# Kernel tuning notes

Measured on AMD Instinct MI355X. Metric: run time of the kernel, lower is better.

Reference implementation:

```python
import jax, jax.numpy as jnp
import numpy as np

N_NODES = 100000


def gcn_conv(x, src, dst, dinv, W, b):
    # PyG GCNConv: h = D^-1/2 (A+I) D^-1/2 (x W) + b
    h = x @ W                                   # [N, out]
    norm = dinv[src] * dinv[dst]                # [E'] edge weights
    msg = norm[:, None] * h[src]                # gather + scale
    agg = jax.ops.segment_sum(msg, dst, num_segments=x.shape[0])
    return agg + b


def setup_inputs() -> dict:
    key = jax.random.key(0)
    ks = jax.random.split(key, 8)
    x = jax.random.normal(ks[0], (N_NODES, 64), dtype=jnp.float32)
    edge_index = jax.random.randint(ks[1], (2, 1600000), 0, N_NODES, dtype=jnp.int32)
    s = 0.1
    return {
        "x": x,
        "edge_index": edge_index,
        "W1": jax.random.normal(ks[2], (64, 64), dtype=jnp.float32) * s,
        "b1": jnp.zeros((64,), dtype=jnp.float32),
        "W2": jax.random.normal(ks[3], (64, 32), dtype=jnp.float32) * s,
        "b2": jnp.zeros((32,), dtype=jnp.float32),
        "W3": jax.random.normal(ks[4], (32, 2), dtype=jnp.float32) * s,
        "b3": jnp.zeros((2,), dtype=jnp.float32),
    }


def reference(x, edge_index, W1, b1, W2, b2, W3, b3):
    n = x.shape[0]
    loop = jnp.arange(n, dtype=edge_index.dtype)
    src = jnp.concatenate([edge_index[0], loop])  # add self-loops
    dst = jnp.concatenate([edge_index[1], loop])
    deg = jax.ops.segment_sum(jnp.ones_like(dst, dtype=x.dtype), dst, num_segments=n)
    dinv = jnp.where(deg > 0, jax.lax.rsqrt(jnp.maximum(deg, 1.0)), 0.0)
    h = jax.nn.relu(gcn_conv(x, src, dst, dinv, W1, b1))
    h = jax.nn.relu(gcn_conv(h, src, dst, dinv, W2, b2))
    return gcn_conv(h, src, dst, dinv, W3, b3)
```

## Files before the change

kernel.cpp:

```cpp
#include <hip/hip_runtime.h>
#include <hip/hip_fp16.h>

#define N_NODES 100000
#define N_EDGES 1600000
#define BSHIFT 9
#define NBUCK ((N_NODES + 511) / 512)
#define BCAP 12288

__global__ void bucket1_kernel(const int* __restrict__ src, const int* __restrict__ dst,
                               int* __restrict__ gbcount, int2* __restrict__ bbuf, int E) {
    __shared__ int hcnt[NBUCK];
    __shared__ int hbase[NBUCK];
    int t = threadIdx.x;
    for (int i = t; i < NBUCK; i += 256) hcnt[i] = 0;
    __syncthreads();
    int e0 = blockIdx.x * 2048 + t;
    int ss[8], dd[8];
#pragma unroll
    for (int u = 0; u < 8; u++) {
        int e = e0 + u * 256;
        if (e < E) {
            ss[u] = src[e];
            dd[u] = dst[e];
            atomicAdd(&hcnt[dd[u] >> BSHIFT], 1);
        } else {
            dd[u] = -1;
        }
    }
    __syncthreads();
    for (int i = t; i < NBUCK; i += 256) {
        int c = hcnt[i];
        hbase[i] = c ? atomicAdd(&gbcount[i], c) : 0;
        hcnt[i] = 0;
    }
    __syncthreads();
#pragma unroll
    for (int u = 0; u < 8; u++) {
        if (dd[u] >= 0) {
            int bk = dd[u] >> BSHIFT;
            int r = atomicAdd(&hcnt[bk], 1);
            bbuf[(size_t)bk * BCAP + hbase[bk] + r] = make_int2(ss[u], dd[u]);
        }
    }
}

__global__ void scan196_kernel(const int* __restrict__ gbcount, int* __restrict__ gbase,
                               int* __restrict__ rowptrN, int E) {
    __shared__ int s[256];
    int t = threadIdx.x;
    int v = (t < NBUCK) ? gbcount[t] : 0;
    s[t] = v;
    __syncthreads();
    for (int off = 1; off < 256; off <<= 1) {
        int u = (t >= off) ? s[t - off] : 0;
        __syncthreads();
        s[t] += u;
        __syncthreads();
    }
    if (t < NBUCK) gbase[t] = s[t] - v;
    if (t == 0) *rowptrN = E;
}

__global__ __launch_bounds__(512)
void bucket2_kernel(const int2* __restrict__ bbuf, const int* __restrict__ gbcount,
                    const int* __restrict__ gbase, int* __restrict__ rowptr,
                    float* __restrict__ dinv, int* __restrict__ eidx, int N) {
    int b = blockIdx.x;
    int base_node = b << BSHIFT;
    int nn = min(512, N - base_node);
    int t = threadIdx.x;
    __shared__ int s[512];
    __shared__ int cur[512];
    s[t] = 0;
    __syncthreads();
    int sz = gbcount[b];
    const int2* eb = bbuf + (size_t)b * BCAP;
    for (int j = t; j < sz; j += 512) atomicAdd(&s[eb[j].y - base_node], 1);
    __syncthreads();
    int myc = s[t];
    if (t < nn) dinv[base_node + t] = rsqrtf((float)myc + 1.0f);
    __syncthreads();
    for (int off = 1; off < 512; off <<= 1) {
        int u = (t >= off) ? s[t - off] : 0;
        __syncthreads();
        s[t] += u;
        __syncthreads();
    }
    int rp = gbase[b] + s[t] - myc;
    if (t < nn) rowptr[base_node + t] = rp;
    cur[t] = rp;
    __syncthreads();
    for (int j = t; j < sz; j += 512) {
        int2 e = eb[j];
        int pos = atomicAdd(&cur[e.y - base_node], 1);
        eidx[pos] = e.x;
    }
}

__global__ void sortrow_wave(const int* __restrict__ rowptr, int* __restrict__ eidx, int n) {
    int g = (blockIdx.x * blockDim.x + threadIdx.x) >> 6;
    int lane = threadIdx.x & 63;
    if (g >= n) return;
    int start = rowptr[g];
    int end = rowptr[g + 1];
    int len = end - start;
    if (len <= 1) return;

    if (len <= 64) {
        int v = (lane < len) ? eidx[start + lane] : 0x7fffffff;
#pragma unroll
        for (int k = 2; k <= 64; k <<= 1) {
#pragma unroll
            for (int j = k >> 1; j > 0; j >>= 1) {
                int partner = __shfl_xor(v, j, 64);
                bool up = ((lane & k) == 0);
                bool keepMin = (((lane & j) == 0) == up);
                int mn = min(v, partner), mx = max(v, partner);
                v = keepMin ? mn : mx;
            }
        }
        if (lane < len) eidx[start + lane] = v;
    } else if (lane == 0) {
        for (int i = start + 1; i < end; i++) {
            int key = eidx[i];
            int j = i - 1;
            while (j >= start && eidx[j] > key) { eidx[j + 1] = eidx[j]; j--; }
            eidx[j + 1] = key;
        }
    }
}

template <int FIN, int FOUT, typename TO>
__global__ __launch_bounds__(256, 2)
void gemm_tiled(const float* __restrict__ in, const float* __restrict__ W,
                const float* __restrict__ dinv, TO* __restrict__ out, int n) {
    constexpr int CG = FOUT / 4;
    constexpr int RG = 256 / CG;
    constexpr int TR = RG * 4;
    constexpr int LDA = FIN + 4;
    __shared__ float sIn[TR * LDA];
    __shared__ float sW[FIN * FOUT];

    for (int i = threadIdx.x; i < FIN * FOUT / 4; i += 256)
        ((float4*)sW)[i] = ((const float4*)W)[i];

    int r0 = blockIdx.x * TR;
    for (int i = threadIdx.x; i < TR * FIN / 4; i += 256) {
        int rr = i / (FIN / 4);
        int cc = i % (FIN / 4);
        int gr = r0 + rr;
        float4 v = (gr < n) ? ((const float4*)in)[(size_t)gr * (FIN / 4) + cc]
                            : make_float4(0.f, 0.f, 0.f, 0.f);
        *(float4*)&sIn[rr * LDA + cc * 4] = v;
    }
    __syncthreads();

    int tc = threadIdx.x % CG;
    int tr = threadIdx.x / CG;
    int rbase = tr * 4, cbase = tc * 4;
    float acc[4][4] = {};

#pragma unroll 2
    for (int k = 0; k < FIN; k += 4) {
        float4 a[4], b[4];
#pragma unroll
        for (int i = 0; i < 4; i++) a[i] = *(float4*)&sIn[(rbase + i) * LDA + k];
#pragma unroll
        for (int kk = 0; kk < 4; kk++) b[kk] = *(float4*)&sW[(k + kk) * FOUT + cbase];
#pragma unroll
        for (int i = 0; i < 4; i++) {
            acc[i][0] += a[i].x * b[0].x + a[i].y * b[1].x + a[i].z * b[2].x + a[i].w * b[3].x;
            acc[i][1] += a[i].x * b[0].y + a[i].y * b[1].y + a[i].z * b[2].y + a[i].w * b[3].y;
            acc[i][2] += a[i].x * b[0].z + a[i].y * b[1].z + a[i].z * b[2].z + a[i].w * b[3].z;
            acc[i][3] += a[i].x * b[0].w + a[i].y * b[1].w + a[i].z * b[2].w + a[i].w * b[3].w;
        }
    }

#pragma unroll
    for (int i = 0; i < 4; i++) {
        int gr = r0 + rbase + i;
        if (gr < n) {
            float dv = dinv[gr];
            if constexpr (sizeof(TO) == 2) {
                union { __half h[4]; uint2 u; } pk;
                pk.h[0] = __float2half_rn(dv * acc[i][0]);
                pk.h[1] = __float2half_rn(dv * acc[i][1]);
                pk.h[2] = __float2half_rn(dv * acc[i][2]);
                pk.h[3] = __float2half_rn(dv * acc[i][3]);
                *(uint2*)&out[(size_t)gr * FOUT + cbase] = pk.u;
            } else {
                *(float4*)&out[(size_t)gr * FOUT + cbase] =
                    make_float4(dv * acc[i][0], dv * acc[i][1], dv * acc[i][2], dv * acc[i][3]);
            }
        }
    }
}

template <int FIN, int FOUT>
__global__ void gemm_kernel(const float* __restrict__ in, const float* __restrict__ W,
                            const float* __restrict__ dinv, float* __restrict__ out, int n) {
    __shared__ float sW[FIN * FOUT];
    for (int i = threadIdx.x; i < FIN * FOUT; i += blockDim.x) sW[i] = W[i];
    __syncthreads();
    constexpr int ROWS = 256 / FOUT;
    int r = blockIdx.x * ROWS + threadIdx.x / FOUT;
    int c = threadIdx.x % FOUT;
    if (r >= n) return;
    float acc = 0.f;
#pragma unroll
    for (int k = 0; k < FIN; k++) acc += in[r * FIN + k] * sW[k * FOUT + c];
    out[r * FOUT + c] = dinv[r] * acc;
}

template <int F, bool RELU>
__global__ void agg_h2_kernel(const int* __restrict__ eidx, const int* __restrict__ rowptr,
                              const float* __restrict__ dinv, const __half2* __restrict__ h2,
                              const float* __restrict__ b, float* __restrict__ out, int n) {
    constexpr int L = F / 2;
    int g = (blockIdx.x * blockDim.x + threadIdx.x) / L;
    int lane = threadIdx.x % L;
    if (g >= n) return;
    int j = rowptr[g];
    int end = rowptr[g + 1];
    float di = dinv[g];
    float2 hs = __half22float2(h2[(size_t)g * L + lane]);

    float2 a0 = {0, 0}, a1 = {0, 0}, a2 = {0, 0}, a3 = {0, 0};
    float2 a4 = {0, 0}, a5 = {0, 0}, a6 = {0, 0}, a7 = {0, 0};
    for (; j + 8 <= end; j += 8) {
        int s0 = eidx[j];
        int s1 = eidx[j + 1];
        int s2 = eidx[j + 2];
        int s3 = eidx[j + 3];
        int s4 = eidx[j + 4];
        int s5 = eidx[j + 5];
        int s6 = eidx[j + 6];
        int s7 = eidx[j + 7];
        float2 v0 = __half22float2(h2[(size_t)s0 * L + lane]);
        float2 v1 = __half22float2(h2[(size_t)s1 * L + lane]);
        float2 v2 = __half22float2(h2[(size_t)s2 * L + lane]);
        float2 v3 = __half22float2(h2[(size_t)s3 * L + lane]);
        float2 v4 = __half22float2(h2[(size_t)s4 * L + lane]);
        float2 v5 = __half22float2(h2[(size_t)s5 * L + lane]);
        float2 v6 = __half22float2(h2[(size_t)s6 * L + lane]);
        float2 v7 = __half22float2(h2[(size_t)s7 * L + lane]);
        a0.x += v0.x; a0.y += v0.y;
        a1.x += v1.x; a1.y += v1.y;
        a2.x += v2.x; a2.y += v2.y;
        a3.x += v3.x; a3.y += v3.y;
        a4.x += v4.x; a4.y += v4.y;
        a5.x += v5.x; a5.y += v5.y;
        a6.x += v6.x; a6.y += v6.y;
        a7.x += v7.x; a7.y += v7.y;
    }
    for (; j + 2 <= end; j += 2) {
        int s0 = eidx[j];
        int s1 = eidx[j + 1];
        float2 v0 = __half22float2(h2[(size_t)s0 * L + lane]);
        float2 v1 = __half22float2(h2[(size_t)s1 * L + lane]);
        a0.x += v0.x; a0.y += v0.y;
        a1.x += v1.x; a1.y += v1.y;
    }
    if (j < end) {
        float2 v = __half22float2(h2[(size_t)eidx[j] * L + lane]);
        a2.x += v.x; a2.y += v.y;
    }
    float ax = ((a0.x + a1.x) + (a2.x + a3.x)) + ((a4.x + a5.x) + (a6.x + a7.x));
    float ay = ((a0.y + a1.y) + (a2.y + a3.y)) + ((a4.y + a5.y) + (a6.y + a7.y));
    float vx = di * (ax + hs.x) + b[2 * lane];
    float vy = di * (ay + hs.y) + b[2 * lane + 1];
    if (RELU) { vx = fmaxf(vx, 0.f); vy = fmaxf(vy, 0.f); }
    *(float2*)&out[(size_t)g * F + 2 * lane] = make_float2(vx, vy);
}

template <int F, bool RELU>
__global__ void agg_kernel(const int* __restrict__ eidx, const int* __restrict__ rowptr,
                           const float* __restrict__ dinv, const float* __restrict__ h,
                           const float* __restrict__ b, float* __restrict__ out, int n) {
    int g = (blockIdx.x * blockDim.x + threadIdx.x) / F;
    int lane = threadIdx.x % F;
    if (g >= n) return;
    int j = rowptr[g];
    int end = rowptr[g + 1];
    float di = dinv[g];
    float hs = h[(size_t)g * F + lane];

    float acc0 = 0.f, acc1 = 0.f, acc2 = 0.f, acc3 = 0.f;
    float acc4 = 0.f, acc5 = 0.f, acc6 = 0.f, acc7 = 0.f;
    for (; j + 8 <= end; j += 8) {
        int s0 = eidx[j];
        int s1 = eidx[j + 1];
        int s2 = eidx[j + 2];
        int s3 = eidx[j + 3];
        int s4 = eidx[j + 4];
        int s5 = eidx[j + 5];
        int s6 = eidx[j + 6];
        int s7 = eidx[j + 7];
        acc0 += h[(size_t)s0 * F + lane];
        acc1 += h[(size_t)s1 * F + lane];
        acc2 += h[(size_t)s2 * F + lane];
        acc3 += h[(size_t)s3 * F + lane];
        acc4 += h[(size_t)s4 * F + lane];
        acc5 += h[(size_t)s5 * F + lane];
        acc6 += h[(size_t)s6 * F + lane];
        acc7 += h[(size_t)s7 * F + lane];
    }
    for (; j + 2 <= end; j += 2) {
        int s0 = eidx[j];
        int s1 = eidx[j + 1];
        acc0 += h[(size_t)s0 * F + lane];
        acc1 += h[(size_t)s1 * F + lane];
    }
    if (j < end) {
        acc2 += h[(size_t)eidx[j] * F + lane];
    }
    float acc = ((acc0 + acc1) + (acc2 + acc3)) + ((acc4 + acc5) + (acc6 + acc7));
    float v = di * (acc + hs) + b[lane];
    out[(size_t)g * F + lane] = RELU ? fmaxf(v, 0.f) : v;
}

extern "C" void kernel_launch(void* const* d_in, const int* in_sizes, int n_in,
                              void* d_out, int out_size, void* d_ws, size_t ws_size,
                              hipStream_t stream) {
    const float* x  = (const float*)d_in[0];
    const int* ei   = (const int*)d_in[1];
    const float* W1 = (const float*)d_in[2];
    const float* b1 = (const float*)d_in[3];
    const float* W2 = (const float*)d_in[4];
    const float* b2 = (const float*)d_in[5];
    const float* W3 = (const float*)d_in[6];
    const float* b3 = (const float*)d_in[7];
    float* out = (float*)d_out;

    const int N = N_NODES;
    const int E = N_EDGES;
    const int* src = ei;
    const int* dst = ei + E;

    char* p = (char*)d_ws;
    int*   rowptr  = (int*)p;             p += ((size_t)(N + 1) * 4 + 15) / 16 * 16;
    float* dinv    = (float*)p;           p += ((size_t)N * 4 + 15) / 16 * 16;
    int*   gbcount = (int*)p;             p += ((size_t)NBUCK * 4 + 15) / 16 * 16;
    int*   gbase   = (int*)p;             p += ((size_t)NBUCK * 4 + 15) / 16 * 16;
    int*   eidx    = (int*)p;             p += (size_t)E * 4;
    __half* A      = (__half*)p;          p += (size_t)N * 64 * 2;
    float* B       = (float*)p;
    int2*  bbuf    = (int2*)B;
    float* A3      = (float*)A;

    const int T = 256;

    hipMemsetAsync(gbcount, 0, NBUCK * sizeof(int), stream);
    bucket1_kernel<<<(E + 2047) / 2048, T, 0, stream>>>(src, dst, gbcount, bbuf, E);
    scan196_kernel<<<1, 256, 0, stream>>>(gbcount, gbase, rowptr + N, E);
    bucket2_kernel<<<NBUCK, 512, 0, stream>>>(bbuf, gbcount, gbase, rowptr, dinv, eidx, N);
    sortrow_wave<<<(N * 64 + T - 1) / T, T, 0, stream>>>(rowptr, eidx, N);

    gemm_tiled<64, 64, __half><<<(N + 63) / 64, T, 0, stream>>>(x, W1, dinv, A, N);
    agg_h2_kernel<64, true><<<(N * 32 + T - 1) / T, T, 0, stream>>>(eidx, rowptr, dinv,
                                                                    (const __half2*)A, b1, B, N);

    gemm_tiled<64, 32, __half><<<(N + 127) / 128, T, 0, stream>>>(B, W2, dinv, A, N);
    agg_h2_kernel<32, true><<<(N * 16 + T - 1) / T, T, 0, stream>>>(eidx, rowptr, dinv,
                                                                    (const __half2*)A, b2, B, N);

    gemm_kernel<32, 2><<<(N + 127) / 128, T, 0, stream>>>(B, W3, dinv, A3, N);
    agg_kernel<2, false><<<(N * 2 + T - 1) / T, T, 0, stream>>>(eidx, rowptr, dinv, A3, b3, out, N);
}
```

Measured before the change: 292.0 us.

## Fuse per-row sort into bucket scatter and vectorize fp16 aggregation gathers

The per-row edge sort moves into the end of bucket2_kernel. Each wave sorts rows using the post-scatter cursor array, so the separate sortrow_wave launch and its rowptr re-reads go away. The aggregation kernels for layers 1 and 2 are replaced by agg_vec_kernel. It uses 8 lanes per node, each loading a wide fp16 vector (16 or 8 bytes) per neighbour instead of one half2 per lane, with two accumulator sets. This cuts the number of load instructions and threads per gather but lowers per-node parallelism, and the fused sort adds serial work to bucket2's blocks.

```diff
diff --git a/kernel.cpp b/kernel.cpp
--- a/kernel.cpp
+++ b/kernel.cpp
@@ -74,6 +74,7 @@
     s[t] = 0;
     __syncthreads();
     int sz = gbcount[b];
+    int gb = gbase[b];
     const int2* eb = bbuf + (size_t)b * BCAP;
     for (int j = t; j < sz; j += 512) atomicAdd(&s[eb[j].y - base_node], 1);
     __syncthreads();
@@ -86,7 +87,7 @@
         s[t] += u;
         __syncthreads();
     }
-    int rp = gbase[b] + s[t] - myc;
+    int rp = gb + s[t] - myc;
     if (t < nn) rowptr[base_node + t] = rp;
     cur[t] = rp;
     __syncthreads();
@@ -95,37 +96,35 @@
         int pos = atomicAdd(&cur[e.y - base_node], 1);
         eidx[pos] = e.x;
     }
-}
-
-__global__ void sortrow_wave(const int* __restrict__ rowptr, int* __restrict__ eidx, int n) {
-    int g = (blockIdx.x * blockDim.x + threadIdx.x) >> 6;
-    int lane = threadIdx.x & 63;
-    if (g >= n) return;
-    int start = rowptr[g];
-    int end = rowptr[g + 1];
-    int len = end - start;
-    if (len <= 1) return;
-
-    if (len <= 64) {
-        int v = (lane < len) ? eidx[start + lane] : 0x7fffffff;
-#pragma unroll
-        for (int k = 2; k <= 64; k <<= 1) {
-#pragma unroll
-            for (int j = k >> 1; j > 0; j >>= 1) {
-                int partner = __shfl_xor(v, j, 64);
-                bool up = ((lane & k) == 0);
-                bool keepMin = (((lane & j) == 0) == up);
-                int mn = min(v, partner), mx = max(v, partner);
-                v = keepMin ? mn : mx;
+    __syncthreads();
+
+    int wid = t >> 6, lane = t & 63;
+    for (int r = wid; r < nn; r += 8) {
+        int start = (r == 0) ? gb : cur[r - 1];
+        int end = cur[r];
+        int len = end - start;
+        if (len <= 1) continue;
+        if (len <= 64) {
+            int v = (lane < len) ? eidx[start + lane] : 0x7fffffff;
+#pragma unroll
+            for (int k = 2; k <= 64; k <<= 1) {
+#pragma unroll
+                for (int j = k >> 1; j > 0; j >>= 1) {
+                    int partner = __shfl_xor(v, j, 64);
+                    bool up = ((lane & k) == 0);
+                    bool keepMin = (((lane & j) == 0) == up);
+                    int mn = min(v, partner), mx = max(v, partner);
+                    v = keepMin ? mn : mx;
+                }
             }
-        }
-        if (lane < len) eidx[start + lane] = v;
-    } else if (lane == 0) {
-        for (int i = start + 1; i < end; i++) {
-            int key = eidx[i];
-            int j = i - 1;
-            while (j >= start && eidx[j] > key) { eidx[j + 1] = eidx[j]; j--; }
-            eidx[j + 1] = key;
+            if (lane < len) eidx[start + lane] = v;
+        } else if (lane == 0) {
+            for (int i = start + 1; i < end; i++) {
+                int key = eidx[i];
+                int j = i - 1;
+                while (j >= start && eidx[j] > key) { eidx[j + 1] = eidx[j]; j--; }
+                eidx[j + 1] = key;
+            }
         }
     }
 }
@@ -213,20 +212,25 @@
 }
 
 template <int F, bool RELU>
-__global__ void agg_h2_kernel(const int* __restrict__ eidx, const int* __restrict__ rowptr,
-                              const float* __restrict__ dinv, const __half2* __restrict__ h2,
-                              const float* __restrict__ b, float* __restrict__ out, int n) {
-    constexpr int L = F / 2;
+__global__ __launch_bounds__(256, 4)
+void agg_vec_kernel(const int* __restrict__ eidx, const int* __restrict__ rowptr,
+                    const float* __restrict__ dinv, const __half* __restrict__ h,
+                    const float* __restrict__ bias, float* __restrict__ out, int n) {
+    constexpr int L = 8;
+    constexpr int PH = F / L;
+    using vh = _Float16 __attribute__((ext_vector_type(PH)));
     int g = (blockIdx.x * blockDim.x + threadIdx.x) / L;
     int lane = threadIdx.x % L;
     if (g >= n) return;
     int j = rowptr[g];
     int end = rowptr[g + 1];
     float di = dinv[g];
-    float2 hs = __half22float2(h2[(size_t)g * L + lane]);
-
-    float2 a0 = {0, 0}, a1 = {0, 0}, a2 = {0, 0}, a3 = {0, 0};
-    float2 a4 = {0, 0}, a5 = {0, 0}, a6 = {0, 0}, a7 = {0, 0};
+    const __half* hb = h + lane * PH;
+
+    float acc0[PH], acc1[PH];
+#pragma unroll
+    for (int q = 0; q < PH; q++) { acc0[q] = 0.f; acc1[q] = 0.f; }
+
     for (; j + 8 <= end; j += 8) {
         int s0 = eidx[j];
         int s1 = eidx[j + 1];
@@ -236,41 +240,47 @@
         int s5 = eidx[j + 5];
         int s6 = eidx[j + 6];
         int s7 = eidx[j + 7];
-        float2 v0 = __half22float2(h2[(size_t)s0 * L + lane]);
-        float2 v1 = __half22float2(h2[(size_t)s1 * L + lane]);
-        float2 v2 = __half22float2(h2[(size_t)s2 * L + lane]);
-        float2 v3 = __half22float2(h2[(size_t)s3 * L + lane]);
-        float2 v4 = __half22float2(h2[(size_t)s4 * L + lane]);
-        float2 v5 = __half22float2(h2[(size_t)s5 * L + lane]);
-        float2 v6 = __half22float2(h2[(size_t)s6 * L + lane]);
-        float2 v7 = __half22float2(h2[(size_t)s7 * L + lane]);
-        a0.x += v0.x; a0.y += v0.y;
-        a1.x += v1.x; a1.y += v1.y;
-        a2.x += v2.x; a2.y += v2.y;
-        a3.x += v3.x; a3.y += v3.y;
-        a4.x += v4.x; a4.y += v4.y;
-        a5.x += v5.x; a5.y += v5.y;
-        a6.x += v6.x; a6.y += v6.y;
-        a7.x += v7.x; a7.y += v7.y;
+        vh v0 = *(const vh*)(hb + (size_t)s0 * F);
+        vh v1 = *(const vh*)(hb + (size_t)s1 * F);
+        vh v2 = *(const vh*)(hb + (size_t)s2 * F);
+        vh v3 = *(const vh*)(hb + (size_t)s3 * F);
+        vh v4 = *(const vh*)(hb + (size_t)s4 * F);
+        vh v5 = *(const vh*)(hb + (size_t)s5 * F);
+        vh v6 = *(const vh*)(hb + (size_t)s6 * F);
+        vh v7 = *(const vh*)(hb + (size_t)s7 * F);
+#pragma unroll
+        for (int q = 0; q < PH; q++) {
+            acc0[q] += (float)v0[q] + (float)v2[q];
+            acc1[q] += (float)v1[q] + (float)v3[q];
+            acc0[q] += (float)v4[q] + (float)v6[q];
+            acc1[q] += (float)v5[q] + (float)v7[q];
+        }
     }
     for (; j + 2 <= end; j += 2) {
         int s0 = eidx[j];
         int s1 = eidx[j + 1];
-        float2 v0 = __half22float2(h2[(size_t)s0 * L + lane]);
-        float2 v1 = __half22float2(h2[(size_t)s1 * L + lane]);
-        a0.x += v0.x; a0.y += v0.y;
-        a1.x += v1.x; a1.y += v1.y;
+        vh v0 = *(const vh*)(hb + (size_t)s0 * F);
+        vh v1 = *(const vh*)(hb + (size_t)s1 * F);
+#pragma unroll
+        for (int q = 0; q < PH; q++) { acc0[q] += (float)v0[q]; acc1[q] += (float)v1[q]; }
     }
     if (j < end) {
-        float2 v = __half22float2(h2[(size_t)eidx[j] * L + lane]);
-        a2.x += v.x; a2.y += v.y;
-    }
-    float ax = ((a0.x + a1.x) + (a2.x + a3.x)) + ((a4.x + a5.x) + (a6.x + a7.x));
-    float ay = ((a0.y + a1.y) + (a2.y + a3.y)) + ((a4.y + a5.y) + (a6.y + a7.y));
-    float vx = di * (ax + hs.x) + b[2 * lane];
-    float vy = di * (ay + hs.y) + b[2 * lane + 1];
-    if (RELU) { vx = fmaxf(vx, 0.f); vy = fmaxf(vy, 0.f); }
-    *(float2*)&out[(size_t)g * F + 2 * lane] = make_float2(vx, vy);
+        vh v = *(const vh*)(hb + (size_t)eidx[j] * F);
+#pragma unroll
+        for (int q = 0; q < PH; q++) acc0[q] += (float)v[q];
+    }
+
+    vh sv = *(const vh*)(hb + (size_t)g * F);
+    float res[PH];
+#pragma unroll
+    for (int q = 0; q < PH; q++) {
+        float v = di * ((acc0[q] + acc1[q]) + (float)sv[q]) + bias[lane * PH + q];
+        res[q] = RELU ? fmaxf(v, 0.f) : v;
+    }
+    float* ob = out + (size_t)g * F + lane * PH;
+#pragma unroll
+    for (int q = 0; q < PH; q += 4)
+        *(float4*)(ob + q) = make_float4(res[q], res[q + 1], res[q + 2], res[q + 3]);
 }
 
 template <int F, bool RELU>
@@ -354,15 +364,12 @@
     bucket1_kernel<<<(E + 2047) / 2048, T, 0, stream>>>(src, dst, gbcount, bbuf, E);
     scan196_kernel<<<1, 256, 0, stream>>>(gbcount, gbase, rowptr + N, E);
     bucket2_kernel<<<NBUCK, 512, 0, stream>>>(bbuf, gbcount, gbase, rowptr, dinv, eidx, N);
-    sortrow_wave<<<(N * 64 + T - 1) / T, T, 0, stream>>>(rowptr, eidx, N);
 
     gemm_tiled<64, 64, __half><<<(N + 63) / 64, T, 0, stream>>>(x, W1, dinv, A, N);
-    agg_h2_kernel<64, true><<<(N * 32 + T - 1) / T, T, 0, stream>>>(eidx, rowptr, dinv,
-                                                                    (const __half2*)A, b1, B, N);
+    agg_vec_kernel<64, true><<<(N * 8 + T - 1) / T, T, 0, stream>>>(eidx, rowptr, dinv, A, b1, B, N);
 
     gemm_tiled<64, 32, __half><<<(N + 127) / 128, T, 0, stream>>>(B, W2, dinv, A, N);
-    agg_h2_kernel<32, true><<<(N * 16 + T - 1) / T, T, 0, stream>>>(eidx, rowptr, dinv,
-                                                                    (const __half2*)A, b2, B, N);
+    agg_vec_kernel<32, true><<<(N * 8 + T - 1) / T, T, 0, stream>>>(eidx, rowptr, dinv, A, b2, B, N);
 
     gemm_kernel<32, 2><<<(N + 127) / 128, T, 0, stream>>>(B, W3, dinv, A3, N);
     agg_kernel<2, false><<<(N * 2 + T - 1) / T, T, 0, stream>>>(eidx, rowptr, dinv, A3, b3, out, N);
```

Measured after the change: 330.5 us. 1.13x slower.
